# Kernel tuning notes

Hardware: AMD Instinct MI355X
Metric: run time of the kernel (lower is better)

The kernel has to match this reference:

```python
import jax, jax.numpy as jnp
import numpy as np

INPUT_DIM = 3072
D_MODEL = 128      # mamba_hidden_dim
EXPAND = 2
D_INNER = EXPAND * D_MODEL   # 256
D_STATE = 16
D_CONV = 4
DT_RANK = D_MODEL // 16      # 8
NUM_LANES = 6
B, L = 4, 2048


def rmsnorm(x, w, eps=1e-5):
    return x * jax.lax.rsqrt(jnp.mean(x * x, axis=-1, keepdims=True) + eps) * w


def mamba_block(x, W_in, conv_w, conv_b, W_x, W_dt, b_dt, A_log, Dp, W_out):
    # x: [B, L, D_MODEL]
    bsz, seqlen, _ = x.shape
    xz = x @ W_in                              # [B, L, 2*D_INNER]
    xs, res = jnp.split(xz, 2, axis=-1)        # each [B, L, D_INNER]

    # depthwise causal conv1d over time
    xc = jnp.transpose(xs, (0, 2, 1))          # [B, C, L]
    k = conv_w[:, None, :]                     # [C, 1, K]
    xc = jax.lax.conv_general_dilated(
        xc, k, window_strides=(1,), padding=[(D_CONV - 1, 0)],
        dimension_numbers=('NCH', 'OIH', 'NCH'), feature_group_count=D_INNER)
    xc = xc + conv_b[None, :, None]
    xs = jax.nn.silu(jnp.transpose(xc, (0, 2, 1)))  # [B, L, C]

    # input-dependent SSM parameters
    dbl = xs @ W_x                             # [B, L, DT_RANK + 2*D_STATE]
    dt = dbl[..., :DT_RANK]
    Bm = dbl[..., DT_RANK:DT_RANK + D_STATE]   # [B, L, S]
    Cm = dbl[..., DT_RANK + D_STATE:]          # [B, L, S]
    delta = jax.nn.softplus(dt @ W_dt + b_dt)  # [B, L, C]

    A = -jnp.exp(A_log)                        # [C, S]
    dA = jnp.exp(delta[..., None] * A)                           # [B, L, C, S]
    dBu = delta[..., None] * Bm[:, :, None, :] * xs[..., None]   # [B, L, C, S]

    def step(h, inp):
        dA_t, dBu_t, C_t = inp                 # [B,C,S], [B,C,S], [B,S]
        h = dA_t * h + dBu_t
        y = jnp.einsum('bcs,bs->bc', h, C_t)
        return h, y

    h0 = jnp.zeros((bsz, D_INNER, D_STATE), x.dtype)
    _, ys = jax.lax.scan(
        step, h0,
        (jnp.moveaxis(dA, 1, 0), jnp.moveaxis(dBu, 1, 0), jnp.moveaxis(Cm, 1, 0)))
    y = jnp.moveaxis(ys, 0, 1) + xs * Dp       # [B, L, C]
    y = y * jax.nn.silu(res)
    return y @ W_out                           # [B, L, D_MODEL]


def setup_inputs() -> dict:
    key = jax.random.key(0)
    ks = jax.random.split(key, 12)
    s = 0.02
    inp = {
        'x': jax.random.normal(ks[0], (B, L, INPUT_DIM), jnp.float32),
        'W_emb': jax.random.normal(ks[1], (INPUT_DIM, D_MODEL), jnp.float32) * s,
        'b_emb': jnp.zeros((D_MODEL,), jnp.float32),
        'norm_w': jnp.ones((D_MODEL,), jnp.float32),
        'W_in': jax.random.normal(ks[2], (D_MODEL, 2 * D_INNER), jnp.float32) * s,
        'conv_w': jax.random.normal(ks[3], (D_INNER, D_CONV), jnp.float32) * 0.1,
        'conv_b': jnp.zeros((D_INNER,), jnp.float32),
        'W_x': jax.random.normal(ks[4], (D_INNER, DT_RANK + 2 * D_STATE), jnp.float32) * s,
        'W_dt': jax.random.normal(ks[5], (DT_RANK, D_INNER), jnp.float32) * s,
        'b_dt': jnp.full((D_INNER,), -2.0, jnp.float32),
        'A_log': jnp.log(jnp.broadcast_to(jnp.arange(1, D_STATE + 1, dtype=jnp.float32), (D_INNER, D_STATE))),
        'Dp': jnp.ones((D_INNER,), jnp.float32),
        'W_out': jax.random.normal(ks[6], (D_INNER, D_MODEL), jnp.float32) * s,
        'normf_w': jnp.ones((D_MODEL,), jnp.float32),
        'W_head': jax.random.normal(ks[7], (D_MODEL, NUM_LANES), jnp.float32) * s,
        'b_head': jnp.zeros((NUM_LANES,), jnp.float32),
    }
    return inp


def reference(x, W_emb, b_emb, norm_w, W_in, conv_w, conv_b, W_x, W_dt, b_dt,
              A_log, Dp, W_out, normf_w, W_head, b_head):
    h = x @ W_emb + b_emb                        # project 3072 -> 128
    h = h + mamba_block(rmsnorm(h, norm_w), W_in, conv_w, conv_b, W_x, W_dt,
                        b_dt, A_log, Dp, W_out)  # residual Mamba block
    Fm = rmsnorm(h, normf_w)
    # dropout is identity in eval
    out = Fm @ W_head + b_head                   # [B, L, NUM_LANES]
    pi = jax.nn.softmax(out, axis=-1)
    lane_preds = jnp.argmax(pi, axis=-1)
    return pi, lane_preds
```

## Files before the change

kernel.cpp:

```cpp
#include <hip/hip_runtime.h>
#include <hip/hip_bf16.h>
#include <math.h>

constexpr int B_ = 4, L_ = 2048, IN_DIM = 3072, DM = 128, DI = 256, DS = 16, NL = 6;
constexpr int ROWS = B_ * L_;
constexpr int SPLITK = 8, KC = IN_DIM / SPLITK;

static __device__ __forceinline__ float silu_f(float x) {
  return x / (1.f + __expf(-x));
}

__global__ __launch_bounds__(256) void gemm_emb_splitk(const float* __restrict__ A,
                                                       const float* __restrict__ Bv,
                                                       float* __restrict__ part) {
  constexpr int BM = 64, BK = 32;
  __shared__ float As[BK][BM + 4];
  __shared__ float Bs[BK][128 + 4];
  int split = blockIdx.x;
  int bm = blockIdx.y * BM;
  int kb = split * KC;
  int tid = threadIdx.x;
  int tm = tid >> 4, tn = tid & 15;
  float acc[4][8] = {};
  for (int k0 = 0; k0 < KC; k0 += BK) {
#pragma unroll
    for (int p = 0; p < 2; ++p) {
      int i = tid + p * 256;
      int r = i >> 3, kq = (i & 7) * 4;
      float4 a4 = *(const float4*)&A[(size_t)(bm + r) * IN_DIM + kb + k0 + kq];
      As[kq + 0][r] = a4.x;
      As[kq + 1][r] = a4.y;
      As[kq + 2][r] = a4.z;
      As[kq + 3][r] = a4.w;
    }
#pragma unroll
    for (int p = 0; p < 4; ++p) {
      int i = tid + p * 256;
      int r = i >> 5, c = (i & 31) * 4;
      *(float4*)&Bs[r][c] = *(const float4*)&Bv[(size_t)(kb + k0 + r) * DM + c];
    }
    __syncthreads();
#pragma unroll
    for (int kk = 0; kk < BK; ++kk) {
      float4 a4 = *(const float4*)&As[kk][tm * 4];
      float4 b0 = *(const float4*)&Bs[kk][tn * 4];
      float4 b1 = *(const float4*)&Bs[kk][64 + tn * 4];
      float a[4] = {a4.x, a4.y, a4.z, a4.w};
      float b[8] = {b0.x, b0.y, b0.z, b0.w, b1.x, b1.y, b1.z, b1.w};
#pragma unroll
      for (int i = 0; i < 4; ++i)
#pragma unroll
        for (int j = 0; j < 8; ++j) acc[i][j] = fmaf(a[i], b[j], acc[i][j]);
    }
    __syncthreads();
  }
#pragma unroll
  for (int i = 0; i < 4; ++i) {
    size_t rowoff = ((size_t)split * ROWS + bm + tm * 4 + i) * DM;
    float4 o0 = {acc[i][0], acc[i][1], acc[i][2], acc[i][3]};
    float4 o1 = {acc[i][4], acc[i][5], acc[i][6], acc[i][7]};
    *(float4*)&part[rowoff + tn * 4] = o0;
    *(float4*)&part[rowoff + 64 + tn * 4] = o1;
  }
}

__global__ __launch_bounds__(256) void reduce_rms_kernel(const float* __restrict__ part,
                                                         const float* __restrict__ b_emb,
                                                         const float* __restrict__ norm_w,
                                                         float* __restrict__ h0,
                                                         float* __restrict__ u) {
  int wave = threadIdx.x >> 6, lane = threadIdx.x & 63;
  int row = blockIdx.x * 4 + wave;
  float sx = 0.f, sy = 0.f;
#pragma unroll
  for (int sp = 0; sp < SPLITK; ++sp) {
    float2 v = *(const float2*)(part + ((size_t)sp * ROWS + row) * DM + 2 * lane);
    sx += v.x;
    sy += v.y;
  }
  float2 be = *(const float2*)(b_emb + 2 * lane);
  sx += be.x;
  sy += be.y;
  float2 hv = {sx, sy};
  *(float2*)(h0 + (size_t)row * DM + 2 * lane) = hv;
  float ss = sx * sx + sy * sy;
#pragma unroll
  for (int o = 32; o >= 1; o >>= 1) ss += __shfl_xor(ss, o);
  float rs = 1.f / sqrtf(ss * (1.f / 128.f) + 1e-5f);
  float2 wv = *(const float2*)(norm_w + 2 * lane);
  float2 o2 = {sx * rs * wv.x, sy * rs * wv.y};
  *(float2*)(u + (size_t)row * DM + 2 * lane) = o2;
}

__global__ __launch_bounds__(256) void gemm_in(const float* __restrict__ A,
                                               const float* __restrict__ Bv,
                                               float* __restrict__ C) {
  constexpr int BM = 64, BK = 32, N = 512;
  __shared__ float As[BK][BM + 4];
  __shared__ float Bs[BK][128 + 4];
  int bn = blockIdx.x * 128;
  int bm = blockIdx.y * BM;
  int tid = threadIdx.x;
  int tm = tid >> 4, tn = tid & 15;
  float acc[4][8] = {};
  for (int k0 = 0; k0 < DM; k0 += BK) {
#pragma unroll
    for (int p = 0; p < 2; ++p) {
      int i = tid + p * 256;
      int r = i >> 3, kq = (i & 7) * 4;
      float4 a4 = *(const float4*)&A[(size_t)(bm + r) * DM + k0 + kq];
      As[kq + 0][r] = a4.x;
      As[kq + 1][r] = a4.y;
      As[kq + 2][r] = a4.z;
      As[kq + 3][r] = a4.w;
    }
#pragma unroll
    for (int p = 0; p < 4; ++p) {
      int i = tid + p * 256;
      int r = i >> 5, c = (i & 31) * 4;
      *(float4*)&Bs[r][c] = *(const float4*)&Bv[(size_t)(k0 + r) * N + bn + c];
    }
    __syncthreads();
#pragma unroll
    for (int kk = 0; kk < BK; ++kk) {
      float4 a4 = *(const float4*)&As[kk][tm * 4];
      float4 b0 = *(const float4*)&Bs[kk][tn * 4];
      float4 b1 = *(const float4*)&Bs[kk][64 + tn * 4];
      float a[4] = {a4.x, a4.y, a4.z, a4.w};
      float b[8] = {b0.x, b0.y, b0.z, b0.w, b1.x, b1.y, b1.z, b1.w};
#pragma unroll
      for (int i = 0; i < 4; ++i)
#pragma unroll
        for (int j = 0; j < 8; ++j) acc[i][j] = fmaf(a[i], b[j], acc[i][j]);
    }
    __syncthreads();
  }
#pragma unroll
  for (int i = 0; i < 4; ++i) {
    size_t rowoff = (size_t)(bm + tm * 4 + i) * N + bn;
    float4 o0 = {acc[i][0], acc[i][1], acc[i][2], acc[i][3]};
    float4 o1 = {acc[i][4], acc[i][5], acc[i][6], acc[i][7]};
    *(float4*)&C[rowoff + tn * 4] = o0;
    *(float4*)&C[rowoff + 64 + tn * 4] = o1;
  }
}

__global__ __launch_bounds__(256) void conv_silu_kernel(const float* __restrict__ xz,
                                                        const float* __restrict__ conv_w,
                                                        const float* __restrict__ conv_b,
                                                        float* __restrict__ xs_row,
                                                        float* __restrict__ xs_T) {
  __shared__ float tile[64][65];
  __shared__ float cw[64][4];
  __shared__ float cb[64];
  int b = blockIdx.z, l0 = blockIdx.y * 64, c0 = blockIdx.x * 64;
  int tid = threadIdx.x;
  cw[tid / 4][tid % 4] = conv_w[(size_t)c0 * 4 + tid];
  if (tid < 64) cb[tid] = conv_b[c0 + tid];
  __syncthreads();
  int cl = tid % 64;
  int lbase = tid / 64;
#pragma unroll
  for (int i = 0; i < 16; ++i) {
    int ll = lbase + 4 * i;
    int l = l0 + ll;
    float acc = cb[cl];
#pragma unroll
    for (int k = 0; k < 4; ++k) {
      int li = l + k - 3;
      if (li >= 0) acc = fmaf(xz[((size_t)(b * L_ + li)) * 512 + c0 + cl], cw[cl][k], acc);
    }
    tile[ll][cl] = silu_f(acc);
  }
  __syncthreads();
  for (int i = tid; i < 4096; i += 256) {
    int lr = i / 64, c = i % 64;
    xs_row[((size_t)(b * L_ + l0 + lr)) * DI + c0 + c] = tile[lr][c];
  }
  for (int i = tid; i < 4096; i += 256) {
    int c = i / 64, lr = i % 64;
    xs_T[((size_t)(b * DI + c0 + c)) * L_ + l0 + lr] = tile[lr][c];
  }
}

__global__ __launch_bounds__(256) void dbl_kernel(const float* __restrict__ xs_row,
                                                  const float* __restrict__ W_x,
                                                  float* __restrict__ dbl) {
  __shared__ float Xs[32][257];
  __shared__ float Wx[256 * 40];
  int tid = threadIdx.x;
  int r0 = blockIdx.x * 32;
  for (int i = tid; i < 32 * 64; i += 256) {
    int r = i >> 6, kq = (i & 63) * 4;
    float4 v = *(const float4*)&xs_row[(size_t)(r0 + r) * DI + kq];
    Xs[r][kq + 0] = v.x;
    Xs[r][kq + 1] = v.y;
    Xs[r][kq + 2] = v.z;
    Xs[r][kq + 3] = v.w;
  }
  for (int i = tid; i < 256 * 40; i += 256) Wx[i] = W_x[i];
  __syncthreads();
  int r = tid & 31, q = tid >> 5;
  float acc[5] = {};
  for (int k = 0; k < 256; ++k) {
    float v = Xs[r][k];
#pragma unroll
    for (int j = 0; j < 5; ++j) acc[j] = fmaf(v, Wx[k * 40 + q * 5 + j], acc[j]);
  }
#pragma unroll
  for (int j = 0; j < 5; ++j) dbl[(size_t)(r0 + r) * 40 + q * 5 + j] = acc[j];
}

__global__ __launch_bounds__(256) void delta_kernel(const float* __restrict__ dbl,
                                                    const float* __restrict__ W_dt,
                                                    const float* __restrict__ b_dt,
                                                    float* __restrict__ delta_T) {
  __shared__ float Tile[32][257];
  __shared__ float Dt[32][8];
  __shared__ float Wdt[8 * 256];
  int tid = threadIdx.x;
  int r0 = blockIdx.x * 32;
  int b = r0 / L_, l0 = r0 % L_;
  if (tid < 256) {
    int r = tid >> 3, k = tid & 7;
    Dt[r][k] = dbl[(size_t)(r0 + r) * 40 + k];
  }
  for (int i = tid; i < 8 * 256; i += 256) Wdt[i] = W_dt[i];
  __syncthreads();
  int c = tid;
  float bd = b_dt[c];
  for (int r = 0; r < 32; ++r) {
    float a = bd;
#pragma unroll
    for (int k = 0; k < 8; ++k) a = fmaf(Dt[r][k], Wdt[k * 256 + c], a);
    float sp = (a > 20.f) ? a : log1pf(__expf(a));
    Tile[r][c] = sp;
  }
  __syncthreads();
  for (int i = tid; i < 32 * 256; i += 256) {
    int cc = i >> 5, rr = i & 31;
    delta_T[((size_t)(b * DI + cc)) * L_ + l0 + rr] = Tile[rr][cc];
  }
}

__global__ __launch_bounds__(512) void scan_kernel(const float* __restrict__ delta_T,
                                                   const float* __restrict__ xs_T,
                                                   const float* __restrict__ dbl,
                                                   const float* __restrict__ A_log,
                                                   const float* __restrict__ Dp,
                                                   const float* __restrict__ xz,
                                                   float* __restrict__ y) {
  __shared__ float s_aprod[32][16];
  __shared__ float s_hend[32][16];
  __shared__ float s_hstart[32][16];
  int tid = threadIdx.x;
  int k = tid >> 4, s = tid & 15;
  int g = blockIdx.x;
  int b = g >> 8, c = g & 255;
  float A = -__expf(A_log[c * DS + s]);
  float dpc = Dp[c];
  const float* dp = delta_T + (size_t)g * L_ + k * 64;
  const float* xp = xs_T + (size_t)g * L_ + k * 64;
  const float* bp = dbl + ((size_t)(b * L_ + k * 64)) * 40 + 8 + s;
  const float* cp = dbl + ((size_t)(b * L_ + k * 64)) * 40 + 24 + s;

  float aprod = 1.f, h = 0.f;
  for (int j = 0; j < 64; j += 4) {
    float4 d4 = *(const float4*)(dp + j);
    float4 x4 = *(const float4*)(xp + j);
    float dj[4] = {d4.x, d4.y, d4.z, d4.w};
    float xj[4] = {x4.x, x4.y, x4.z, x4.w};
#pragma unroll
    for (int u = 0; u < 4; ++u) {
      float Bv = bp[(size_t)(j + u) * 40];
      float dA = __expf(dj[u] * A);
      aprod *= dA;
      h = fmaf(dA, h, dj[u] * Bv * xj[u]);
    }
  }
  s_aprod[k][s] = aprod;
  s_hend[k][s] = h;
  __syncthreads();

  if (tid < 16) {
    float hh = 0.f;
    for (int kk = 0; kk < 32; ++kk) {
      s_hstart[kk][tid] = hh;
      hh = fmaf(s_aprod[kk][tid], hh, s_hend[kk][tid]);
    }
  }
  __syncthreads();

  h = s_hstart[k][s];
  float* yp = y + ((size_t)(b * L_) + k * 64) * DI + c;
  const float* rp = xz + ((size_t)(b * L_) + k * 64) * 512 + 256 + c;
  for (int j = 0; j < 64; j += 4) {
    float4 d4 = *(const float4*)(dp + j);
    float4 x4 = *(const float4*)(xp + j);
    float dj[4] = {d4.x, d4.y, d4.z, d4.w};
    float xj[4] = {x4.x, x4.y, x4.z, x4.w};
#pragma unroll
    for (int u = 0; u < 4; ++u) {
      float Bv = bp[(size_t)(j + u) * 40];
      float Cv = cp[(size_t)(j + u) * 40];
      float dA = __expf(dj[u] * A);
      h = fmaf(dA, h, dj[u] * Bv * xj[u]);
      float p = h * Cv;
      p += __shfl_xor(p, 8, 16);
      p += __shfl_xor(p, 4, 16);
      p += __shfl_xor(p, 2, 16);
      p += __shfl_xor(p, 1, 16);
      if (s == 0) {
        float res = rp[(size_t)(j + u) * 512];
        yp[(size_t)(j + u) * DI] = (p + xj[u] * dpc) * silu_f(res);
      }
    }
  }
}

__global__ __launch_bounds__(256) void final_gemm_kernel(const float* __restrict__ y,
                                                         const float* __restrict__ W_out,
                                                         const float* __restrict__ h0,
                                                         const float* __restrict__ normf_w,
                                                         const float* __restrict__ W_head,
                                                         const float* __restrict__ b_head,
                                                         float* __restrict__ pi_out,
                                                         float* __restrict__ pred_out) {
  constexpr int BM = 32, BK = 32;
  __shared__ float As[BK][BM + 4];
  __shared__ float Bs[BK][128 + 4];
  __shared__ float Wh[128 * 6];
  int tid = threadIdx.x;
  int tm = tid >> 4, tn = tid & 15;
  int bm = blockIdx.x * BM;
  for (int i = tid; i < 768; i += 256) Wh[i] = W_head[i];
  float acc[2][8] = {};
  for (int k0 = 0; k0 < DI; k0 += BK) {
    {
      int r = tid >> 3, kq = (tid & 7) * 4;
      float4 a4 = *(const float4*)&y[(size_t)(bm + r) * DI + k0 + kq];
      As[kq + 0][r] = a4.x;
      As[kq + 1][r] = a4.y;
      As[kq + 2][r] = a4.z;
      As[kq + 3][r] = a4.w;
    }
#pragma unroll
    for (int p = 0; p < 4; ++p) {
      int i = tid + p * 256;
      int r = i >> 5, c = (i & 31) * 4;
      *(float4*)&Bs[r][c] = *(const float4*)&W_out[(size_t)(k0 + r) * DM + c];
    }
    __syncthreads();
#pragma unroll
    for (int kk = 0; kk < BK; ++kk) {
      float a0 = As[kk][tm * 2], a1 = As[kk][tm * 2 + 1];
      float4 b0 = *(const float4*)&Bs[kk][tn * 4];
      float4 b1 = *(const float4*)&Bs[kk][64 + tn * 4];
      float b[8] = {b0.x, b0.y, b0.z, b0.w, b1.x, b1.y, b1.z, b1.w};
#pragma unroll
      for (int j = 0; j < 8; ++j) acc[0][j] = fmaf(a0, b[j], acc[0][j]);
#pragma unroll
      for (int j = 0; j < 8; ++j) acc[1][j] = fmaf(a1, b[j], acc[1][j]);
    }
    __syncthreads();
  }
  float4 nwa = *(const float4*)&normf_w[tn * 4];
  float4 nwb = *(const float4*)&normf_w[64 + tn * 4];
  float nw[8] = {nwa.x, nwa.y, nwa.z, nwa.w, nwb.x, nwb.y, nwb.z, nwb.w};
  float bh[6];
#pragma unroll
  for (int j = 0; j < 6; ++j) bh[j] = b_head[j];
#pragma unroll
  for (int i = 0; i < 2; ++i) {
    int row = bm + tm * 2 + i;
    float4 h0a = *(const float4*)&h0[(size_t)row * DM + tn * 4];
    float4 h0b = *(const float4*)&h0[(size_t)row * DM + 64 + tn * 4];
    float hv[8] = {acc[i][0] + h0a.x, acc[i][1] + h0a.y, acc[i][2] + h0a.z, acc[i][3] + h0a.w,
                   acc[i][4] + h0b.x, acc[i][5] + h0b.y, acc[i][6] + h0b.z, acc[i][7] + h0b.w};
    float ss = 0.f;
#pragma unroll
    for (int j = 0; j < 8; ++j) ss += hv[j] * hv[j];
    ss += __shfl_xor(ss, 1);
    ss += __shfl_xor(ss, 2);
    ss += __shfl_xor(ss, 4);
    ss += __shfl_xor(ss, 8);
    float rs = 1.f / sqrtf(ss * (1.f / 128.f) + 1e-5f);
    float lg[6] = {};
#pragma unroll
    for (int j = 0; j < 8; ++j) {
      float fm = hv[j] * rs * nw[j];
      int col = (j < 4) ? (tn * 4 + j) : (64 + tn * 4 + (j - 4));
#pragma unroll
      for (int l = 0; l < 6; ++l) lg[l] = fmaf(fm, Wh[col * 6 + l], lg[l]);
    }
#pragma unroll
    for (int l = 0; l < 6; ++l) {
      lg[l] += __shfl_xor(lg[l], 1);
      lg[l] += __shfl_xor(lg[l], 2);
      lg[l] += __shfl_xor(lg[l], 4);
      lg[l] += __shfl_xor(lg[l], 8);
      lg[l] += bh[l];
    }
    if (tn == 0) {
      float mv = lg[0];
      int am = 0;
#pragma unroll
      for (int l = 1; l < 6; ++l)
        if (lg[l] > mv) { mv = lg[l]; am = l; }
      float e[6], sum = 0.f;
#pragma unroll
      for (int l = 0; l < 6; ++l) { e[l] = __expf(lg[l] - mv); sum += e[l]; }
      float inv = 1.f / sum;
#pragma unroll
      for (int l = 0; l < 6; ++l) pi_out[(size_t)row * NL + l] = e[l] * inv;
      pred_out[row] = (float)am;
    }
  }
}

extern "C" void kernel_launch(void* const* d_in, const int* in_sizes, int n_in,
                              void* d_out, int out_size, void* d_ws, size_t ws_size,
                              hipStream_t stream) {
  const float* x = (const float*)d_in[0];
  const float* W_emb = (const float*)d_in[1];
  const float* b_emb = (const float*)d_in[2];
  const float* norm_w = (const float*)d_in[3];
  const float* W_in = (const float*)d_in[4];
  const float* conv_w = (const float*)d_in[5];
  const float* conv_b = (const float*)d_in[6];
  const float* W_x = (const float*)d_in[7];
  const float* W_dt = (const float*)d_in[8];
  const float* b_dt = (const float*)d_in[9];
  const float* A_log = (const float*)d_in[10];
  const float* Dp = (const float*)d_in[11];
  const float* W_out = (const float*)d_in[12];
  const float* normf_w = (const float*)d_in[13];
  const float* W_head = (const float*)d_in[14];
  const float* b_head = (const float*)d_in[15];

  float* ws = (float*)d_ws;
  float* h0 = ws;
  float* u = h0 + 1048576;
  float* xz = u + 1048576;
  float* xs_row = xz + 4194304;
  float* xs_T = xs_row + 2097152;
  float* dbl = xs_T + 2097152;
  float* delta_T = dbl + 327680;
  float* y = delta_T + 2097152;

  float* part = xz;

  float* pi_out = (float*)d_out;
  float* pred_out = pi_out + (size_t)ROWS * NL;

  gemm_emb_splitk<<<dim3(SPLITK, ROWS / 64), 256, 0, stream>>>(x, W_emb, part);
  reduce_rms_kernel<<<ROWS / 4, 256, 0, stream>>>(part, b_emb, norm_w, h0, u);
  gemm_in<<<dim3(4, 128), 256, 0, stream>>>(u, W_in, xz);
  conv_silu_kernel<<<dim3(4, 32, 4), 256, 0, stream>>>(xz, conv_w, conv_b, xs_row, xs_T);
  dbl_kernel<<<256, 256, 0, stream>>>(xs_row, W_x, dbl);
  delta_kernel<<<256, 256, 0, stream>>>(dbl, W_dt, b_dt, delta_T);
  scan_kernel<<<1024, 512, 0, stream>>>(delta_T, xs_T, dbl, A_log, Dp, xz, y);
  final_gemm_kernel<<<256, 256, 0, stream>>>(y, W_out, h0, normf_w, W_head, b_head, pi_out, pred_out);
}
```

Measured before the change: 406.4 us.

## Prefetch GEMM tiles into registers, shrink GEMM row tiles, raise split-K

Adds register-level software prefetching to the embedding, in-projection and final GEMMs. Each kernel now loads the next K tile into registers while it computes on the current shared-memory tile, and the trailing barrier is dropped. The in-projection and final GEMMs use half-height row tiles, doubling their grid sizes to raise occupancy and parallelism. Split-K for the embedding GEMM goes from 8 to 12, which adds blocks but also more partial-sum traffic and a larger workspace footprint for the partials. The prefetch registers may also raise register pressure.

```diff
diff --git a/kernel.cpp b/kernel.cpp
--- a/kernel.cpp
+++ b/kernel.cpp
@@ -4,7 +4,7 @@
 
 constexpr int B_ = 4, L_ = 2048, IN_DIM = 3072, DM = 128, DI = 256, DS = 16, NL = 6;
 constexpr int ROWS = B_ * L_;
-constexpr int SPLITK = 8, KC = IN_DIM / SPLITK;
+constexpr int SPLITK = 12, KC = IN_DIM / SPLITK;
 
 static __device__ __forceinline__ float silu_f(float x) {
   return x / (1.f + __expf(-x));
@@ -21,25 +21,43 @@
   int kb = split * KC;
   int tid = threadIdx.x;
   int tm = tid >> 4, tn = tid & 15;
+
+  float4 pa[2], pb[4];
+#define EMB_PRELOAD(K0)                                                                  \
+  {                                                                                      \
+    _Pragma("unroll") for (int p = 0; p < 2; ++p) {                                      \
+      int i = tid + p * 256;                                                             \
+      int r = i >> 3, kq = (i & 7) * 4;                                                  \
+      pa[p] = *(const float4*)&A[(size_t)(bm + r) * IN_DIM + kb + (K0) + kq];            \
+    }                                                                                    \
+    _Pragma("unroll") for (int p = 0; p < 4; ++p) {                                      \
+      int i = tid + p * 256;                                                             \
+      int r = i >> 5, c = (i & 31) * 4;                                                  \
+      pb[p] = *(const float4*)&Bv[(size_t)(kb + (K0) + r) * DM + c];                     \
+    }                                                                                    \
+  }
+
   float acc[4][8] = {};
+  EMB_PRELOAD(0);
   for (int k0 = 0; k0 < KC; k0 += BK) {
+    __syncthreads();
 #pragma unroll
     for (int p = 0; p < 2; ++p) {
       int i = tid + p * 256;
       int r = i >> 3, kq = (i & 7) * 4;
-      float4 a4 = *(const float4*)&A[(size_t)(bm + r) * IN_DIM + kb + k0 + kq];
-      As[kq + 0][r] = a4.x;
-      As[kq + 1][r] = a4.y;
-      As[kq + 2][r] = a4.z;
-      As[kq + 3][r] = a4.w;
+      As[kq + 0][r] = pa[p].x;
+      As[kq + 1][r] = pa[p].y;
+      As[kq + 2][r] = pa[p].z;
+      As[kq + 3][r] = pa[p].w;
     }
 #pragma unroll
     for (int p = 0; p < 4; ++p) {
       int i = tid + p * 256;
       int r = i >> 5, c = (i & 31) * 4;
-      *(float4*)&Bs[r][c] = *(const float4*)&Bv[(size_t)(kb + k0 + r) * DM + c];
+      *(float4*)&Bs[r][c] = pb[p];
     }
     __syncthreads();
+    if (k0 + BK < KC) EMB_PRELOAD(k0 + BK);
 #pragma unroll
     for (int kk = 0; kk < BK; ++kk) {
       float4 a4 = *(const float4*)&As[kk][tm * 4];
@@ -52,8 +70,8 @@
 #pragma unroll
         for (int j = 0; j < 8; ++j) acc[i][j] = fmaf(a[i], b[j], acc[i][j]);
     }
-    __syncthreads();
-  }
+  }
+#undef EMB_PRELOAD
 #pragma unroll
   for (int i = 0; i < 4; ++i) {
     size_t rowoff = ((size_t)split * ROWS + bm + tm * 4 + i) * DM;
@@ -95,49 +113,61 @@
 __global__ __launch_bounds__(256) void gemm_in(const float* __restrict__ A,
                                                const float* __restrict__ Bv,
                                                float* __restrict__ C) {
-  constexpr int BM = 64, BK = 32, N = 512;
-  __shared__ float As[BK][BM + 4];
+  constexpr int BK = 32, N = 512;
+  __shared__ float As[BK][32 + 4];
   __shared__ float Bs[BK][128 + 4];
   int bn = blockIdx.x * 128;
-  int bm = blockIdx.y * BM;
+  int bm = blockIdx.y * 32;
   int tid = threadIdx.x;
   int tm = tid >> 4, tn = tid & 15;
-  float acc[4][8] = {};
+
+  float4 pa, pb[4];
+#define IN_PRELOAD(K0)                                                                   \
+  {                                                                                      \
+    int r = tid >> 3, kq = (tid & 7) * 4;                                                \
+    pa = *(const float4*)&A[(size_t)(bm + r) * DM + (K0) + kq];                          \
+    _Pragma("unroll") for (int p = 0; p < 4; ++p) {                                      \
+      int i = tid + p * 256;                                                             \
+      int rr = i >> 5, c = (i & 31) * 4;                                                 \
+      pb[p] = *(const float4*)&Bv[(size_t)((K0) + rr) * N + bn + c];                     \
+    }                                                                                    \
+  }
+
+  float acc[2][8] = {};
+  IN_PRELOAD(0);
   for (int k0 = 0; k0 < DM; k0 += BK) {
-#pragma unroll
-    for (int p = 0; p < 2; ++p) {
-      int i = tid + p * 256;
-      int r = i >> 3, kq = (i & 7) * 4;
-      float4 a4 = *(const float4*)&A[(size_t)(bm + r) * DM + k0 + kq];
-      As[kq + 0][r] = a4.x;
-      As[kq + 1][r] = a4.y;
-      As[kq + 2][r] = a4.z;
-      As[kq + 3][r] = a4.w;
+    __syncthreads();
+    {
+      int r = tid >> 3, kq = (tid & 7) * 4;
+      As[kq + 0][r] = pa.x;
+      As[kq + 1][r] = pa.y;
+      As[kq + 2][r] = pa.z;
+      As[kq + 3][r] = pa.w;
     }
 #pragma unroll
     for (int p = 0; p < 4; ++p) {
       int i = tid + p * 256;
-      int r = i >> 5, c = (i & 31) * 4;
-      *(float4*)&Bs[r][c] = *(const float4*)&Bv[(size_t)(k0 + r) * N + bn + c];
+      int rr = i >> 5, c = (i & 31) * 4;
+      *(float4*)&Bs[rr][c] = pb[p];
     }
     __syncthreads();
+    if (k0 + BK < DM) IN_PRELOAD(k0 + BK);
 #pragma unroll
     for (int kk = 0; kk < BK; ++kk) {
-      float4 a4 = *(const float4*)&As[kk][tm * 4];
+      float2 a2 = *(const float2*)&As[kk][tm * 2];
       float4 b0 = *(const float4*)&Bs[kk][tn * 4];
       float4 b1 = *(const float4*)&Bs[kk][64 + tn * 4];
-      float a[4] = {a4.x, a4.y, a4.z, a4.w};
       float b[8] = {b0.x, b0.y, b0.z, b0.w, b1.x, b1.y, b1.z, b1.w};
 #pragma unroll
-      for (int i = 0; i < 4; ++i)
-#pragma unroll
-        for (int j = 0; j < 8; ++j) acc[i][j] = fmaf(a[i], b[j], acc[i][j]);
-    }
-    __syncthreads();
-  }
-#pragma unroll
-  for (int i = 0; i < 4; ++i) {
-    size_t rowoff = (size_t)(bm + tm * 4 + i) * N + bn;
+      for (int j = 0; j < 8; ++j) acc[0][j] = fmaf(a2.x, b[j], acc[0][j]);
+#pragma unroll
+      for (int j = 0; j < 8; ++j) acc[1][j] = fmaf(a2.y, b[j], acc[1][j]);
+    }
+  }
+#undef IN_PRELOAD
+#pragma unroll
+  for (int i = 0; i < 2; ++i) {
+    size_t rowoff = (size_t)(bm + tm * 2 + i) * N + bn;
     float4 o0 = {acc[i][0], acc[i][1], acc[i][2], acc[i][3]};
     float4 o1 = {acc[i][4], acc[i][5], acc[i][6], acc[i][7]};
     *(float4*)&C[rowoff + tn * 4] = o0;
@@ -326,95 +356,107 @@
                                                          const float* __restrict__ b_head,
                                                          float* __restrict__ pi_out,
                                                          float* __restrict__ pred_out) {
-  constexpr int BM = 32, BK = 32;
-  __shared__ float As[BK][BM + 4];
+  constexpr int BK = 32;
+  __shared__ float As[BK][16 + 4];
   __shared__ float Bs[BK][128 + 4];
   __shared__ float Wh[128 * 6];
   int tid = threadIdx.x;
   int tm = tid >> 4, tn = tid & 15;
-  int bm = blockIdx.x * BM;
+  int bm = blockIdx.x * 16;
   for (int i = tid; i < 768; i += 256) Wh[i] = W_head[i];
-  float acc[2][8] = {};
+
+  float4 pa, pb[4];
+#define FN_PRELOAD(K0)                                                                   \
+  {                                                                                      \
+    if (tid < 128) {                                                                     \
+      int r = tid >> 3, kq = (tid & 7) * 4;                                              \
+      pa = *(const float4*)&y[(size_t)(bm + r) * DI + (K0) + kq];                        \
+    }                                                                                    \
+    _Pragma("unroll") for (int p = 0; p < 4; ++p) {                                      \
+      int i = tid + p * 256;                                                             \
+      int rr = i >> 5, c = (i & 31) * 4;                                                 \
+      pb[p] = *(const float4*)&W_out[(size_t)((K0) + rr) * DM + c];                      \
+    }                                                                                    \
+  }
+
+  float acc[8] = {};
+  FN_PRELOAD(0);
   for (int k0 = 0; k0 < DI; k0 += BK) {
-    {
+    __syncthreads();
+    if (tid < 128) {
       int r = tid >> 3, kq = (tid & 7) * 4;
-      float4 a4 = *(const float4*)&y[(size_t)(bm + r) * DI + k0 + kq];
-      As[kq + 0][r] = a4.x;
-      As[kq + 1][r] = a4.y;
-      As[kq + 2][r] = a4.z;
-      As[kq + 3][r] = a4.w;
+      As[kq + 0][r] = pa.x;
+      As[kq + 1][r] = pa.y;
+      As[kq + 2][r] = pa.z;
+      As[kq + 3][r] = pa.w;
     }
 #pragma unroll
     for (int p = 0; p < 4; ++p) {
       int i = tid + p * 256;
-      int r = i >> 5, c = (i & 31) * 4;
-      *(float4*)&Bs[r][c] = *(const float4*)&W_out[(size_t)(k0 + r) * DM + c];
+      int rr = i >> 5, c = (i & 31) * 4;
+      *(float4*)&Bs[rr][c] = pb[p];
     }
     __syncthreads();
+    if (k0 + BK < DI) FN_PRELOAD(k0 + BK);
 #pragma unroll
     for (int kk = 0; kk < BK; ++kk) {
-      float a0 = As[kk][tm * 2], a1 = As[kk][tm * 2 + 1];
+      float a0 = As[kk][tm];
       float4 b0 = *(const float4*)&Bs[kk][tn * 4];
       float4 b1 = *(const float4*)&Bs[kk][64 + tn * 4];
       float b[8] = {b0.x, b0.y, b0.z, b0.w, b1.x, b1.y, b1.z, b1.w};
 #pragma unroll
-      for (int j = 0; j < 8; ++j) acc[0][j] = fmaf(a0, b[j], acc[0][j]);
-#pragma unroll
-      for (int j = 0; j < 8; ++j) acc[1][j] = fmaf(a1, b[j], acc[1][j]);
-    }
-    __syncthreads();
-  }
+      for (int j = 0; j < 8; ++j) acc[j] = fmaf(a0, b[j], acc[j]);
+    }
+  }
+#undef FN_PRELOAD
   float4 nwa = *(const float4*)&normf_w[tn * 4];
   float4 nwb = *(const float4*)&normf_w[64 + tn * 4];
   float nw[8] = {nwa.x, nwa.y, nwa.z, nwa.w, nwb.x, nwb.y, nwb.z, nwb.w};
   float bh[6];
 #pragma unroll
   for (int j = 0; j < 6; ++j) bh[j] = b_head[j];
-#pragma unroll
-  for (int i = 0; i < 2; ++i) {
-    int row = bm + tm * 2 + i;
-    float4 h0a = *(const float4*)&h0[(size_t)row * DM + tn * 4];
-    float4 h0b = *(const float4*)&h0[(size_t)row * DM + 64 + tn * 4];
-    float hv[8] = {acc[i][0] + h0a.x, acc[i][1] + h0a.y, acc[i][2] + h0a.z, acc[i][3] + h0a.w,
-                   acc[i][4] + h0b.x, acc[i][5] + h0b.y, acc[i][6] + h0b.z, acc[i][7] + h0b.w};
-    float ss = 0.f;
-#pragma unroll
-    for (int j = 0; j < 8; ++j) ss += hv[j] * hv[j];
-    ss += __shfl_xor(ss, 1);
-    ss += __shfl_xor(ss, 2);
-    ss += __shfl_xor(ss, 4);
-    ss += __shfl_xor(ss, 8);
-    float rs = 1.f / sqrtf(ss * (1.f / 128.f) + 1e-5f);
-    float lg[6] = {};
-#pragma unroll
-    for (int j = 0; j < 8; ++j) {
-      float fm = hv[j] * rs * nw[j];
-      int col = (j < 4) ? (tn * 4 + j) : (64 + tn * 4 + (j - 4));
-#pragma unroll
-      for (int l = 0; l < 6; ++l) lg[l] = fmaf(fm, Wh[col * 6 + l], lg[l]);
-    }
-#pragma unroll
-    for (int l = 0; l < 6; ++l) {
-      lg[l] += __shfl_xor(lg[l], 1);
-      lg[l] += __shfl_xor(lg[l], 2);
-      lg[l] += __shfl_xor(lg[l], 4);
-      lg[l] += __shfl_xor(lg[l], 8);
-      lg[l] += bh[l];
-    }
-    if (tn == 0) {
-      float mv = lg[0];
-      int am = 0;
-#pragma unroll
-      for (int l = 1; l < 6; ++l)
-        if (lg[l] > mv) { mv = lg[l]; am = l; }
-      float e[6], sum = 0.f;
-#pragma unroll
-      for (int l = 0; l < 6; ++l) { e[l] = __expf(lg[l] - mv); sum += e[l]; }
-      float inv = 1.f / sum;
-#pragma unroll
-      for (int l = 0; l < 6; ++l) pi_out[(size_t)row * NL + l] = e[l] * inv;
-      pred_out[row] = (float)am;
-    }
+  int row = bm + tm;
+  float4 h0a = *(const float4*)&h0[(size_t)row * DM + tn * 4];
+  float4 h0b = *(const float4*)&h0[(size_t)row * DM + 64 + tn * 4];
+  float hv[8] = {acc[0] + h0a.x, acc[1] + h0a.y, acc[2] + h0a.z, acc[3] + h0a.w,
+                 acc[4] + h0b.x, acc[5] + h0b.y, acc[6] + h0b.z, acc[7] + h0b.w};
+  float ss = 0.f;
+#pragma unroll
+  for (int j = 0; j < 8; ++j) ss += hv[j] * hv[j];
+  ss += __shfl_xor(ss, 1);
+  ss += __shfl_xor(ss, 2);
+  ss += __shfl_xor(ss, 4);
+  ss += __shfl_xor(ss, 8);
+  float rs = 1.f / sqrtf(ss * (1.f / 128.f) + 1e-5f);
+  float lg[6] = {};
+#pragma unroll
+  for (int j = 0; j < 8; ++j) {
+    float fm = hv[j] * rs * nw[j];
+    int col = (j < 4) ? (tn * 4 + j) : (64 + tn * 4 + (j - 4));
+#pragma unroll
+    for (int l = 0; l < 6; ++l) lg[l] = fmaf(fm, Wh[col * 6 + l], lg[l]);
+  }
+#pragma unroll
+  for (int l = 0; l < 6; ++l) {
+    lg[l] += __shfl_xor(lg[l], 1);
+    lg[l] += __shfl_xor(lg[l], 2);
+    lg[l] += __shfl_xor(lg[l], 4);
+    lg[l] += __shfl_xor(lg[l], 8);
+    lg[l] += bh[l];
+  }
+  if (tn == 0) {
+    float mv = lg[0];
+    int am = 0;
+#pragma unroll
+    for (int l = 1; l < 6; ++l)
+      if (lg[l] > mv) { mv = lg[l]; am = l; }
+    float e[6], sum = 0.f;
+#pragma unroll
+    for (int l = 0; l < 6; ++l) { e[l] = __expf(lg[l] - mv); sum += e[l]; }
+    float inv = 1.f / sum;
+#pragma unroll
+    for (int l = 0; l < 6; ++l) pi_out[(size_t)row * NL + l] = e[l] * inv;
+    pred_out[row] = (float)am;
   }
 }
 
@@ -455,10 +497,10 @@
 
   gemm_emb_splitk<<<dim3(SPLITK, ROWS / 64), 256, 0, stream>>>(x, W_emb, part);
   reduce_rms_kernel<<<ROWS / 4, 256, 0, stream>>>(part, b_emb, norm_w, h0, u);
-  gemm_in<<<dim3(4, 128), 256, 0, stream>>>(u, W_in, xz);
+  gemm_in<<<dim3(4, 256), 256, 0, stream>>>(u, W_in, xz);
   conv_silu_kernel<<<dim3(4, 32, 4), 256, 0, stream>>>(xz, conv_w, conv_b, xs_row, xs_T);
   dbl_kernel<<<256, 256, 0, stream>>>(xs_row, W_x, dbl);
   delta_kernel<<<256, 256, 0, stream>>>(dbl, W_dt, b_dt, delta_T);
   scan_kernel<<<1024, 512, 0, stream>>>(delta_T, xs_T, dbl, A_log, Dp, xz, y);
-  final_gemm_kernel<<<256, 256, 0, stream>>>(y, W_out, h0, normf_w, W_head, b_head, pi_out, pred_out);
-}
+  final_gemm_kernel<<<512, 256, 0, stream>>>(y, W_out, h0, normf_w, W_head, b_head, pi_out, pred_out);
+}
```

Result: slower. 446.2 us (+9.8%).

## Use split-bf16 MFMA for the embedding GEMM instead of FP32 FMA

Applied to the files above, without the earlier changes.

Replaces the scalar FP32 embedding GEMM (8192x3072x128) with MFMA bf16 16x16x32 instructions. Each operand is split into a high and a low bf16 part, and three MFMAs per tile (hi*hi, hi*lo, lo*hi) approximate FP32 accuracy. A pre-pass kernel splits and transposes W_emb into hi/lo bf16 buffers stored in the delta_T workspace, and the activations are split on the fly while loading into shared memory. This adds an extra kernel launch and some error from the dropped lo*lo term, in exchange for matrix-core throughput on the largest GEMM.

```diff
diff --git a/kernel.cpp b/kernel.cpp
--- a/kernel.cpp
+++ b/kernel.cpp
@@ -6,61 +6,101 @@
 constexpr int ROWS = B_ * L_;
 constexpr int SPLITK = 8, KC = IN_DIM / SPLITK;
 
+typedef __attribute__((ext_vector_type(8))) short short8b;
+typedef __attribute__((ext_vector_type(4))) float f32x4;
+
 static __device__ __forceinline__ float silu_f(float x) {
   return x / (1.f + __expf(-x));
 }
 
-__global__ __launch_bounds__(256) void gemm_emb_splitk(const float* __restrict__ A,
-                                                       const float* __restrict__ Bv,
-                                                       float* __restrict__ part) {
-  constexpr int BM = 64, BK = 32;
-  __shared__ float As[BK][BM + 4];
-  __shared__ float Bs[BK][128 + 4];
+static __device__ __forceinline__ unsigned short f2bf_rne(float v) {
+  unsigned u = __float_as_uint(v);
+  unsigned r = u + 0x7FFFu + ((u >> 16) & 1u);
+  return (unsigned short)(r >> 16);
+}
+
+__global__ __launch_bounds__(256) void wsplit_kernel(const float* __restrict__ W,
+                                                     unsigned short* __restrict__ wt_hi,
+                                                     unsigned short* __restrict__ wt_lo) {
+  int tid = threadIdx.x;
+  int c = tid & 127;
+  int kc = blockIdx.x * 16 + (tid >> 7) * 8;
+  short8b vh, vl;
+#pragma unroll
+  for (int j = 0; j < 8; ++j) {
+    float v = W[(size_t)(kc + j) * DM + c];
+    unsigned short h = f2bf_rne(v);
+    float hf = __uint_as_float((unsigned)h << 16);
+    vh[j] = (short)h;
+    vl[j] = (short)f2bf_rne(v - hf);
+  }
+  *(short8b*)&wt_hi[(size_t)c * IN_DIM + kc] = vh;
+  *(short8b*)&wt_lo[(size_t)c * IN_DIM + kc] = vl;
+}
+
+__global__ __launch_bounds__(256) void gemm_emb_mfma(const float* __restrict__ A,
+                                                     const unsigned short* __restrict__ wt_hi,
+                                                     const unsigned short* __restrict__ wt_lo,
+                                                     float* __restrict__ part) {
+  constexpr int BM = 64, BK = 32, LDA = 40;
+  __shared__ unsigned short Ah[BM][LDA], Al[BM][LDA];
+  __shared__ unsigned short Bh[DM][LDA], Bl[DM][LDA];
   int split = blockIdx.x;
   int bm = blockIdx.y * BM;
   int kb = split * KC;
   int tid = threadIdx.x;
-  int tm = tid >> 4, tn = tid & 15;
-  float acc[4][8] = {};
+  int w = tid >> 6, l = tid & 63;
+  int fr = l & 15, fk = (l >> 4) * 8;
+
+  f32x4 acc[8] = {};
+
   for (int k0 = 0; k0 < KC; k0 += BK) {
-#pragma unroll
-    for (int p = 0; p < 2; ++p) {
-      int i = tid + p * 256;
-      int r = i >> 3, kq = (i & 7) * 4;
-      float4 a4 = *(const float4*)&A[(size_t)(bm + r) * IN_DIM + kb + k0 + kq];
-      As[kq + 0][r] = a4.x;
-      As[kq + 1][r] = a4.y;
-      As[kq + 2][r] = a4.z;
-      As[kq + 3][r] = a4.w;
-    }
-#pragma unroll
-    for (int p = 0; p < 4; ++p) {
-      int i = tid + p * 256;
-      int r = i >> 5, c = (i & 31) * 4;
-      *(float4*)&Bs[r][c] = *(const float4*)&Bv[(size_t)(kb + k0 + r) * DM + c];
+    {
+      int r = tid >> 2, kq = (tid & 3) * 8;
+      const float* src = &A[(size_t)(bm + r) * IN_DIM + kb + k0 + kq];
+      float4 v0 = *(const float4*)src;
+      float4 v1 = *(const float4*)(src + 4);
+      float vv[8] = {v0.x, v0.y, v0.z, v0.w, v1.x, v1.y, v1.z, v1.w};
+      short8b vh, vl;
+#pragma unroll
+      for (int j = 0; j < 8; ++j) {
+        unsigned short h = f2bf_rne(vv[j]);
+        float hf = __uint_as_float((unsigned)h << 16);
+        vh[j] = (short)h;
+        vl[j] = (short)f2bf_rne(vv[j] - hf);
+      }
+      *(short8b*)&Ah[r][kq] = vh;
+      *(short8b*)&Al[r][kq] = vl;
+    }
+    {
+      int c = tid >> 1, kq = (tid & 1) * 16;
+      const unsigned short* sh = &wt_hi[(size_t)c * IN_DIM + kb + k0 + kq];
+      const unsigned short* sl = &wt_lo[(size_t)c * IN_DIM + kb + k0 + kq];
+      *(short8b*)&Bh[c][kq] = *(const short8b*)sh;
+      *(short8b*)&Bh[c][kq + 8] = *(const short8b*)(sh + 8);
+      *(short8b*)&Bl[c][kq] = *(const short8b*)sl;
+      *(short8b*)&Bl[c][kq + 8] = *(const short8b*)(sl + 8);
     }
     __syncthreads();
-#pragma unroll
-    for (int kk = 0; kk < BK; ++kk) {
-      float4 a4 = *(const float4*)&As[kk][tm * 4];
-      float4 b0 = *(const float4*)&Bs[kk][tn * 4];
-      float4 b1 = *(const float4*)&Bs[kk][64 + tn * 4];
-      float a[4] = {a4.x, a4.y, a4.z, a4.w};
-      float b[8] = {b0.x, b0.y, b0.z, b0.w, b1.x, b1.y, b1.z, b1.w};
-#pragma unroll
-      for (int i = 0; i < 4; ++i)
-#pragma unroll
-        for (int j = 0; j < 8; ++j) acc[i][j] = fmaf(a[i], b[j], acc[i][j]);
+    short8b ah = *(short8b*)&Ah[16 * w + fr][fk];
+    short8b al = *(short8b*)&Al[16 * w + fr][fk];
+#pragma unroll
+    for (int t = 0; t < 8; ++t) {
+      short8b bh = *(short8b*)&Bh[16 * t + fr][fk];
+      short8b bl = *(short8b*)&Bl[16 * t + fr][fk];
+      acc[t] = __builtin_amdgcn_mfma_f32_16x16x32_bf16(ah, bh, acc[t], 0, 0, 0);
+      acc[t] = __builtin_amdgcn_mfma_f32_16x16x32_bf16(ah, bl, acc[t], 0, 0, 0);
+      acc[t] = __builtin_amdgcn_mfma_f32_16x16x32_bf16(al, bh, acc[t], 0, 0, 0);
     }
     __syncthreads();
   }
-#pragma unroll
-  for (int i = 0; i < 4; ++i) {
-    size_t rowoff = ((size_t)split * ROWS + bm + tm * 4 + i) * DM;
-    float4 o0 = {acc[i][0], acc[i][1], acc[i][2], acc[i][3]};
-    float4 o1 = {acc[i][4], acc[i][5], acc[i][6], acc[i][7]};
-    *(float4*)&part[rowoff + tn * 4] = o0;
-    *(float4*)&part[rowoff + 64 + tn * 4] = o1;
+  int orow = bm + 16 * w + (l >> 4) * 4;
+#pragma unroll
+  for (int t = 0; t < 8; ++t) {
+#pragma unroll
+    for (int r = 0; r < 4; ++r) {
+      part[((size_t)split * ROWS + orow + r) * DM + 16 * t + fr] = acc[t][r];
+    }
   }
 }
 
@@ -233,8 +273,7 @@
     float a = bd;
 #pragma unroll
     for (int k = 0; k < 8; ++k) a = fmaf(Dt[r][k], Wdt[k * 256 + c], a);
-    float sp = (a > 20.f) ? a : log1pf(__expf(a));
-    Tile[r][c] = sp;
+    Tile[r][c] = (a > 20.f) ? a : log1pf(__expf(a));
   }
   __syncthreads();
   for (int i = tid; i < 32 * 256; i += 256) {
@@ -449,11 +488,14 @@
   float* y = delta_T + 2097152;
 
   float* part = xz;
+  unsigned short* wt_hi = (unsigned short*)delta_T;
+  unsigned short* wt_lo = wt_hi + (size_t)IN_DIM * DM;
 
   float* pi_out = (float*)d_out;
   float* pred_out = pi_out + (size_t)ROWS * NL;
 
-  gemm_emb_splitk<<<dim3(SPLITK, ROWS / 64), 256, 0, stream>>>(x, W_emb, part);
+  wsplit_kernel<<<192, 256, 0, stream>>>(W_emb, wt_hi, wt_lo);
+  gemm_emb_mfma<<<dim3(SPLITK, ROWS / 64), 256, 0, stream>>>(x, wt_hi, wt_lo, part);
   reduce_rms_kernel<<<ROWS / 4, 256, 0, stream>>>(part, b_emb, norm_w, h0, u);
   gemm_in<<<dim3(4, 128), 256, 0, stream>>>(u, W_in, xz);
   conv_silu_kernel<<<dim3(4, 32, 4), 256, 0, stream>>>(xz, conv_w, conv_b, xs_row, xs_T);
```

Result: faster. 377.5 us (-7.1%).
